# Performance work log

Measured on AMD Instinct MI355X. Metric: run time of the kernel, lower is better.

Reference implementation:

```python
import jax, jax.numpy as jnp
import numpy as np
from math import factorial, sqrt, pi

MAX_DEG = 4
CUTOFF = 5.0

# ---------- Clebsch-Gordan coefficients for real spherical harmonics ----------

def _cg_complex(j1, m1, j2, m2, j3, m3):
    if m1 + m2 != m3 or j3 < abs(j1 - j2) or j3 > j1 + j2:
        return 0.0
    f = factorial
    pre = sqrt((2 * j3 + 1) * f(j1 + j2 - j3) * f(j1 - j2 + j3) * f(-j1 + j2 + j3) / f(j1 + j2 + j3 + 1))
    pre *= sqrt(f(j1 + m1) * f(j1 - m1) * f(j2 + m2) * f(j2 - m2) * f(j3 + m3) * f(j3 - m3))
    s = 0.0
    for k in range(0, j1 + j2 + j3 + 1):
        t = [k, j1 + j2 - j3 - k, j1 - m1 - k, j2 + m2 - k, j3 - j2 + m1 + k, j3 - j1 - m2 + k]
        if min(t) < 0:
            continue
        s += (-1) ** k / (f(t[0]) * f(t[1]) * f(t[2]) * f(t[3]) * f(t[4]) * f(t[5]))
    return pre * s


def _u_matrix(l):
    # complex->real spherical-harmonic change of basis, U[m_real+l, mu+l]
    U = np.zeros((2 * l + 1, 2 * l + 1), dtype=np.complex128)
    U[l, l] = 1.0
    inv_sqrt2 = 1.0 / sqrt(2.0)
    for m in range(1, l + 1):
        U[l + m, l + m] = ((-1) ** m) * inv_sqrt2
        U[l + m, l - m] = inv_sqrt2
        U[l - m, l - m] = 1j * inv_sqrt2
        U[l - m, l + m] = -1j * ((-1) ** m) * inv_sqrt2
    return U


def _real_cg(l1, l2, l3):
    C = np.zeros((2 * l1 + 1, 2 * l2 + 1, 2 * l3 + 1), dtype=np.complex128)
    for m1 in range(-l1, l1 + 1):
        for m2 in range(-l2, l2 + 1):
            m3 = m1 + m2
            if -l3 <= m3 <= l3:
                C[m1 + l1, m2 + l2, m3 + l3] = _cg_complex(l1, m1, l2, m2, l3, m3)
    R = np.einsum('ai,bj,ck,ijk->abc', _u_matrix(l1), _u_matrix(l2), _u_matrix(l3).conj(), C)
    return np.real(R).astype(np.float32)

# Parity-even coupling paths (l1+l2+l3 even), all degrees <= MAX_DEG -> 42 paths
CG_PATHS = []
for _l1 in range(MAX_DEG + 1):
    for _l2 in range(MAX_DEG + 1):
        for _l3 in range(abs(_l1 - _l2), min(MAX_DEG, _l1 + _l2) + 1):
            if (_l1 + _l2 + _l3) % 2 == 0:
                CG_PATHS.append((_l1, _l2, _l3, _real_cg(_l1, _l2, _l3)))
NUM_PATHS = len(CG_PATHS)  # 42


def _sl(l):
    return slice(l * l, (l + 1) * (l + 1))


def tensor_product(x1, x2, w):
    # x1, x2: (E, 1, 25, F); w: (NUM_PATHS, F). One learnable weight per path per channel.
    blocks = [None] * (MAX_DEG + 1)
    for p, (l1, l2, l3, cg) in enumerate(CG_PATHS):
        a = x1[..., _sl(l1), :]
        b = x2[..., _sl(l2), :]
        c = jnp.einsum('...if,...jf,ijk->...kf', a, b, jnp.asarray(cg)) * w[p]
        blocks[l3] = c if blocks[l3] is None else blocks[l3] + c
    return jnp.concatenate(blocks, axis=-2)


def real_sph(u):
    # u: (E,3) unit vectors -> (E, 25) real orthonormal spherical harmonics, index l*l+l+m
    x, y, z = u[..., 0], u[..., 1], u[..., 2]
    L = MAX_DEG
    Cm = [jnp.ones_like(x)]
    Sm = [jnp.zeros_like(x)]
    for m in range(1, L + 1):
        Cm.append(x * Cm[m - 1] - y * Sm[m - 1])
        Sm.append(x * Sm[m - 1] + y * Cm[m - 1])
    Q = {(0, 0): jnp.ones_like(z)}
    for m in range(L + 1):
        if m > 0:
            Q[(m, m)] = (2 * m - 1) * Q[(m - 1, m - 1)]
        if m + 1 <= L:
            Q[(m + 1, m)] = (2 * m + 1) * z * Q[(m, m)]
        for l in range(m + 2, L + 1):
            Q[(l, m)] = ((2 * l - 1) * z * Q[(l - 1, m)] - (l + m - 1) * Q[(l - 2, m)]) / (l - m)
    ys = []
    for l in range(L + 1):
        row = [None] * (2 * l + 1)
        row[l] = sqrt((2 * l + 1) / (4 * pi)) * Q[(l, 0)]
        for m in range(1, l + 1):
            Klm = sqrt((2 * l + 1) / (4 * pi) * factorial(l - m) / factorial(l + m))
            base = sqrt(2.0) * Klm * Q[(l, m)]
            row[l + m] = base * Cm[m]
            row[l - m] = base * Sm[m]
        ys.extend(row)
    return jnp.stack(ys, axis=-1)


def bond_basis(disp, cutoff, num):
    # sinc radial basis * cosine cutoff * spherical harmonics -> (E, 1, 25, num)
    r = jnp.sqrt(jnp.sum(disp * disp, axis=-1) + 1e-12)
    Y = real_sph(disp / r[..., None])  # (E, 25)
    k = jnp.arange(1, num + 1, dtype=disp.dtype)
    rad = jnp.sinc(r[..., None] * k / cutoff)  # (E, num)
    cut = jnp.where(r < cutoff, 0.5 * (1.0 + jnp.cos(np.float32(np.pi) * r / cutoff)), 0.0)
    out = Y[..., :, None] * rad[..., None, :] * cut[..., None, None]
    return out[:, None, :, :]


def setup_inputs() -> dict:
    key = jax.random.key(0)
    k1, k2, k3, k4, k5, k6 = jax.random.split(key, 6)
    N, E, F = 10000, 160000, 16
    return {
        'atomic_descriptors': jax.random.normal(k1, (N, 1, 25, F), dtype=jnp.float32),
        'neighbour_displacements': jax.random.normal(k2, (E, 3), dtype=jnp.float32),
        'weights1': jax.random.normal(k3, (NUM_PATHS, F), dtype=jnp.float32),
        'weights2': jax.random.normal(k4, (NUM_PATHS, F), dtype=jnp.float32),
        'neighbours_i': jax.random.randint(k5, (E,), 0, N, dtype=jnp.int32),
        'neighbours_j': jax.random.randint(k6, (E,), 0, N, dtype=jnp.int32),
    }


def reference(atomic_descriptors, neighbour_displacements, weights1, weights2, neighbours_i, neighbours_j):
    F = atomic_descriptors.shape[-1]
    a1 = atomic_descriptors[neighbours_i]  # (E,1,25,F) irregular gather
    a2 = atomic_descriptors[neighbours_j]
    y = tensor_product(a1, a2, weights1)  # first equivariant CG tensor product
    bexp = bond_basis(neighbour_displacements, CUTOFF, F)  # radial x angular bond basis
    return tensor_product(y, bexp, weights2)
```

## Files before the change

### kernel.cpp

```cpp
#include <hip/hip_runtime.h>

namespace cg {

constexpr double FACT[16] = {
  1.0, 1.0, 2.0, 6.0, 24.0, 120.0, 720.0, 5040.0, 40320.0, 362880.0,
  3628800.0, 39916800.0, 479001600.0, 6227020800.0, 87178291200.0,
  1307674368000.0 };

constexpr double csqrt_(double x){
  if (x <= 0.0) return 0.0;
  double xx = x, g = 1.0;
  while (xx >= 256.0)      { xx *= (1.0/256.0); g *= 16.0;       }
  while (xx >= 4.0)        { xx *= 0.25;        g *= 2.0;        }
  while (xx < (1.0/256.0)) { xx *= 256.0;       g *= (1.0/16.0); }
  while (xx < 1.0)         { xx *= 4.0;         g *= 0.5;        }
  double s = 1.5;
  for (int i = 0; i < 10; ++i) s = 0.5*(s + xx/s);
  return g*s;
}

constexpr double cg_complex(int j1,int m1,int j2,int m2,int j3,int m3){
  if (m1+m2 != m3) return 0.0;
  int dj = j1-j2; if (dj < 0) dj = -dj;
  if (j3 < dj || j3 > j1+j2) return 0.0;
  if (m1<-j1||m1>j1||m2<-j2||m2>j2||m3<-j3||m3>j3) return 0.0;
  double pre = csqrt_((2.0*j3+1.0)*FACT[j1+j2-j3]*FACT[j1-j2+j3]*FACT[-j1+j2+j3]/FACT[j1+j2+j3+1]);
  pre *= csqrt_(FACT[j1+m1]*FACT[j1-m1]*FACT[j2+m2]*FACT[j2-m2]*FACT[j3+m3]*FACT[j3-m3]);
  double s = 0.0;
  for (int k = 0; k <= j1+j2+j3; ++k){
    int t1=j1+j2-j3-k, t2=j1-m1-k, t3=j2+m2-k, t4=j3-j2+m1+k, t5=j3-j1-m2+k;
    if (t1<0||t2<0||t3<0||t4<0||t5<0) continue;
    double term = 1.0/(FACT[k]*FACT[t1]*FACT[t2]*FACT[t3]*FACT[t4]*FACT[t5]);
    s += (k & 1) ? -term : term;
  }
  return pre*s;
}

struct URow { int n; int col[2]; double re[2]; double im[2]; };

constexpr URow urow(int l, int a){
  URow r{};
  const double is2 = 0.70710678118654752440;
  int m = a - l;
  if (m == 0){
    r.n = 1; r.col[0] = l; r.re[0] = 1.0; r.im[0] = 0.0;
  } else if (m > 0){
    r.n = 2;
    r.col[0] = l+m; r.re[0] = (m & 1) ? -is2 : is2; r.im[0] = 0.0;
    r.col[1] = l-m; r.re[1] = is2;                  r.im[1] = 0.0;
  } else {
    int mm = -m; r.n = 2;
    r.col[0] = l-mm; r.re[0] = 0.0; r.im[0] = is2;
    r.col[1] = l+mm; r.re[1] = 0.0; r.im[1] = (mm & 1) ? is2 : -is2;
  }
  return r;
}

struct PTab {
  int nnz;
  unsigned char ia[192];
  unsigned char jb[192];
  unsigned char kc[192];
  float v[192];
};

constexpr PTab build_path(int l1, int l2, int l3){
  double Cc[9][9] = {};
  for (int i = 0; i < 2*l1+1; ++i)
    for (int j = 0; j < 2*l2+1; ++j){
      int m3 = (i-l1)+(j-l2);
      Cc[i][j] = (m3 >= -l3 && m3 <= l3)
               ? cg_complex(l1, i-l1, l2, j-l2, l3, m3) : 0.0;
    }
  PTab t{};
  for (int a = 0; a < 2*l1+1; ++a)
    for (int b = 0; b < 2*l2+1; ++b)
      for (int c = 0; c < 2*l3+1; ++c){
        URow ra = urow(l1,a), rb = urow(l2,b), rc = urow(l3,c);
        double re = 0.0;
        for (int x = 0; x < ra.n; ++x)
          for (int yy = 0; yy < rb.n; ++yy){
            double pr = ra.re[x]*rb.re[yy] - ra.im[x]*rb.im[yy];
            double pi = ra.re[x]*rb.im[yy] + ra.im[x]*rb.re[yy];
            for (int z = 0; z < rc.n; ++z){
              if (rc.col[z]-l3 != (ra.col[x]-l1)+(rb.col[yy]-l2)) continue;
              double ure = pr*rc.re[z] + pi*rc.im[z];
              re += ure * Cc[ra.col[x]][rb.col[yy]];
            }
          }
        if (re > 1e-10 || re < -1e-10){
          t.ia[t.nnz] = (unsigned char)a;
          t.jb[t.nnz] = (unsigned char)b;
          t.kc[t.nnz] = (unsigned char)c;
          t.v[t.nnz]  = (float)re;
          t.nnz++;
        }
      }
  return t;
}

constexpr double PI_D = 3.14159265358979323846264338327950288;
constexpr double Kd(int l, int m){
  double v = csqrt_((2.0*l+1.0)/(4.0*PI_D)*FACT[l-m]/FACT[l+m]);
  if (m) v *= csqrt_(2.0);
  return v;
}

}

#define PATHS_X(X) \
  X(0,0,0,0) X(1,0,1,1) X(2,0,2,2) X(3,0,3,3) X(4,0,4,4) \
  X(5,1,0,1) X(6,1,1,0) X(7,1,1,2) X(8,1,2,1) X(9,1,2,3) X(10,1,3,2) X(11,1,3,4) X(12,1,4,3) \
  X(13,2,0,2) X(14,2,1,1) X(15,2,1,3) X(16,2,2,0) X(17,2,2,2) X(18,2,2,4) X(19,2,3,1) X(20,2,3,3) X(21,2,4,2) X(22,2,4,4) \
  X(23,3,0,3) X(24,3,1,2) X(25,3,1,4) X(26,3,2,1) X(27,3,2,3) X(28,3,3,0) X(29,3,3,2) X(30,3,3,4) X(31,3,4,1) X(32,3,4,3) \
  X(33,4,0,4) X(34,4,1,3) X(35,4,2,2) X(36,4,2,4) X(37,4,3,1) X(38,4,3,3) X(39,4,4,0) X(40,4,4,2) X(41,4,4,4)

#define DECL_TAB(P,L1,L2,L3) static constexpr cg::PTab CGT_##P = cg::build_path(L1,L2,L3);
PATHS_X(DECL_TAB)
#undef DECL_TAB

struct GTab {
  int n;
  int ptot;
  unsigned int zmask;
  unsigned char i8[512], j8[512], kk[512];
  bool np[512], ft[512];
  float v[512];
};

constexpr GTab merge_group(int npaths,
                           const cg::PTab* t0, int l30,
                           const cg::PTab* t1, int l31,
                           const cg::PTab* t2, int l32){
  GTab g{};
  const cg::PTab* ts[3] = {t0, t1, t2};
  int ls[3] = {l30, l31, l32};
  int pofs[3] = {0,0,0};
  int acc = 0;
  for (int s = 0; s < npaths; ++s){ pofs[s] = acc; acc += 2*ls[s]+1; }
  g.ptot = acc;
  bool touched[32] = {};
  for (int j = 0; j < 9; ++j)
    for (int i = 0; i < 9; ++i){
      bool first = true;
      for (int s = 0; s < npaths; ++s){
        const cg::PTab* T = ts[s];
        for (int t = 0; t < T->nnz; ++t){
          if ((int)T->ia[t] == i && (int)T->jb[t] == j){
            int kx = pofs[s] + (int)T->kc[t];
            g.i8[g.n] = (unsigned char)i;
            g.j8[g.n] = (unsigned char)j;
            g.kk[g.n] = (unsigned char)kx;
            g.np[g.n] = first; first = false;
            g.ft[g.n] = !touched[kx]; touched[kx] = true;
            g.v[g.n]  = T->v[t];
            g.n++;
          }
        }
      }
    }
  unsigned int zm = 0;
  for (int k = 0; k < g.ptot; ++k) if (!touched[k]) zm |= (1u << k);
  g.zmask = zm;
  return g;
}

#define GROUPS_X(X) \
  X(0,0, 1,  0,0,   0,0,   0,0) \
  X(0,1, 1,  1,1,   1,1,   1,1) \
  X(0,2, 1,  2,2,   2,2,   2,2) \
  X(0,3, 1,  3,3,   3,3,   3,3) \
  X(0,4, 1,  4,4,   4,4,   4,4) \
  X(1,0, 1,  5,1,   5,1,   5,1) \
  X(1,1, 2,  6,0,   7,2,   7,2) \
  X(1,2, 2,  8,1,   9,3,   9,3) \
  X(1,3, 2, 10,2,  11,4,  11,4) \
  X(1,4, 1, 12,3,  12,3,  12,3) \
  X(2,0, 1, 13,2,  13,2,  13,2) \
  X(2,1, 2, 14,1,  15,3,  15,3) \
  X(2,2, 3, 16,0,  17,2,  18,4) \
  X(2,3, 2, 19,1,  20,3,  20,3) \
  X(2,4, 2, 21,2,  22,4,  22,4) \
  X(3,0, 1, 23,3,  23,3,  23,3) \
  X(3,1, 2, 24,2,  25,4,  25,4) \
  X(3,2, 2, 26,1,  27,3,  27,3) \
  X(3,3, 3, 28,0,  29,2,  30,4) \
  X(3,4, 2, 31,1,  32,3,  32,3) \
  X(4,0, 1, 33,4,  33,4,  33,4) \
  X(4,1, 1, 34,3,  34,3,  34,3) \
  X(4,2, 2, 35,2,  36,4,  36,4) \
  X(4,3, 2, 37,1,  38,3,  38,3) \
  X(4,4, 3, 39,0,  40,2,  41,4)

#define DECL_GROUP(L1,L2,NP,P0,L30,P1,L31,P2,L32) \
  static constexpr GTab G_##L1##_##L2 = \
    merge_group(NP, &CGT_##P0, L30, &CGT_##P1, L31, &CGT_##P2, L32);
GROUPS_X(DECL_GROUP)
#undef DECL_GROUP

static constexpr float K00=(float)cg::Kd(0,0);
static constexpr float K10=(float)cg::Kd(1,0), K11=(float)cg::Kd(1,1);
static constexpr float K20=(float)cg::Kd(2,0), K21=(float)cg::Kd(2,1), K22=(float)cg::Kd(2,2);
static constexpr float K30=(float)cg::Kd(3,0), K31=(float)cg::Kd(3,1), K32=(float)cg::Kd(3,2), K33=(float)cg::Kd(3,3);
static constexpr float K40=(float)cg::Kd(4,0), K41=(float)cg::Kd(4,1), K42=(float)cg::Kd(4,2), K43=(float)cg::Kd(4,3), K44=(float)cg::Kd(4,4);

static constexpr float PI_F = 3.14159274101257324f;

#define RUN_GROUP(GN,L1,L2,NP,P0,L30,P1,L31,P2,L32,S1,S2,DST,WEX) { \
    float part[GN.ptot]; \
    _Pragma("unroll") \
    for (int k = 0; k < GN.ptot; ++k) if ((GN.zmask >> k) & 1u) part[k] = 0.f; \
    float prod = 0.f; \
    _Pragma("unroll") \
    for (int t = 0; t < GN.n; ++t) { \
      if (GN.np[t]) prod = S1[(L1)*(L1)+(int)GN.i8[t]] * S2[(L2)*(L2)+(int)GN.j8[t]]; \
      if (GN.ft[t]) part[GN.kk[t]]  = GN.v[t] * prod; \
      else          part[GN.kk[t]] += GN.v[t] * prod; \
    } \
    { const float wp = WEX(P0); \
      _Pragma("unroll") for (int k = 0; k < 2*(L30)+1; ++k) \
        DST[(L30)*(L30)+k] += wp * part[k]; } \
    if constexpr ((NP) > 1) { const float wp = WEX(P1); \
      _Pragma("unroll") for (int k = 0; k < 2*(L31)+1; ++k) \
        DST[(L31)*(L31)+k] += wp * part[2*(L30)+1 + k]; } \
    if constexpr ((NP) > 2) { const float wp = WEX(P2); \
      _Pragma("unroll") for (int k = 0; k < 2*(L32)+1; ++k) \
        DST[(L32)*(L32)+k] += wp * part[2*(L30)+1 + 2*(L31)+1 + k]; } \
  }

#define TP1W(P) (W1[(P)*16 + f])
#define TP2W(P) (s * W2[(P)*16 + f])

#define TP1_G(L1,L2,NP,P0,L30,P1,L31,P2,L32) \
  RUN_GROUP(G_##L1##_##L2, L1,L2,NP,P0,L30,P1,L31,P2,L32, a1,a2,y,TP1W)
#define TP2_G(L1,L2,NP,P0,L30,P1,L31,P2,L32) \
  RUN_GROUP(G_##L1##_##L2, L1,L2,NP,P0,L30,P1,L31,P2,L32, y,Ys,o,TP2W)

__global__ __launch_bounds__(256)
__attribute__((amdgpu_waves_per_eu(4, 4)))
void bctmd_kernel(
    const float* __restrict__ A,
    const float* __restrict__ D,
    const float* __restrict__ W1,
    const float* __restrict__ W2,
    const int*   __restrict__ NI,
    const int*   __restrict__ NJ,
    float* __restrict__ out,
    int E)
{
  int g = blockIdx.x * 256 + threadIdx.x;
  int e = g >> 4;
  int f = g & 15;
  if (e >= E) return;

  const float* __restrict__ a1p = A + (size_t)NI[e] * 400 + f;
  const float* __restrict__ a2p = A + (size_t)NJ[e] * 400 + f;

  float a1[25], a2[25];
#pragma unroll
  for (int i = 0; i < 25; ++i) a1[i] = a1p[i*16];
#pragma unroll
  for (int i = 0; i < 25; ++i) a2[i] = a2p[i*16];
#pragma unroll
  for (int i = 0; i < 25; ++i) { asm volatile("" : "+v"(a1[i])); }
#pragma unroll
  for (int i = 0; i < 25; ++i) { asm volatile("" : "+v"(a2[i])); }

  float y[25];
#pragma unroll
  for (int i = 0; i < 25; ++i) y[i] = 0.f;
  GROUPS_X(TP1_G)

  float dx = D[3*e], dy = D[3*e+1], dz = D[3*e+2];
  float r2 = dx*dx + dy*dy + dz*dz + 1e-12f;
  float inv = __builtin_amdgcn_rsqf(r2);
  float r   = r2 * inv;
  float ux = dx*inv, uy = dy*inv, uz = dz*inv;

  float Ys[25];
  {
    float C1 = ux,            S1 = uy;
    float C2 = ux*C1 - uy*S1, S2 = ux*S1 + uy*C1;
    float C3 = ux*C2 - uy*S2, S3 = ux*S2 + uy*C2;
    float C4 = ux*C3 - uy*S3, S4 = ux*S3 + uy*C3;
    float z = uz;
    float Q00 = 1.f;
    float Q11 = 1.f, Q22 = 3.f, Q33 = 15.f, Q44 = 105.f;
    float Q10 = z, Q21 = 3.f*z, Q32 = 15.f*z, Q43 = 105.f*z;
    float Q20 = 0.5f*(3.f*z*Q10 - Q00);
    float Q31 = 0.5f*(5.f*z*Q21 - 3.f*Q11);
    float Q42 = 0.5f*(7.f*z*Q32 - 5.f*Q22);
    float Q30 = (5.f*z*Q20 - 2.f*Q10)*(1.f/3.f);
    float Q41 = (7.f*z*Q31 - 4.f*Q21)*(1.f/3.f);
    float Q40 = 0.25f*(7.f*z*Q30 - 3.f*Q20);

    Ys[0]  = K00*Q00;
    Ys[1]  = K11*Q11*S1;  Ys[2]  = K10*Q10;     Ys[3]  = K11*Q11*C1;
    Ys[4]  = K22*Q22*S2;  Ys[5]  = K21*Q21*S1;  Ys[6]  = K20*Q20;
    Ys[7]  = K21*Q21*C1;  Ys[8]  = K22*Q22*C2;
    Ys[9]  = K33*Q33*S3;  Ys[10] = K32*Q32*S2;  Ys[11] = K31*Q31*S1;
    Ys[12] = K30*Q30;     Ys[13] = K31*Q31*C1;  Ys[14] = K32*Q32*C2;
    Ys[15] = K33*Q33*C3;
    Ys[16] = K44*Q44*S4;  Ys[17] = K43*Q43*S3;  Ys[18] = K42*Q42*S2;
    Ys[19] = K41*Q41*S1;  Ys[20] = K40*Q40;     Ys[21] = K41*Q41*C1;
    Ys[22] = K42*Q42*C2;  Ys[23] = K43*Q43*C3;  Ys[24] = K44*Q44*C4;
  }

  float base = PI_F * r * 0.2f;
  float tt  = base * (float)(f+1);
  float rad = __sinf(tt) * __builtin_amdgcn_rcpf(tt);
  float cut = (r < 5.0f) ? 0.5f*(1.0f + __cosf(base)) : 0.0f;
  float s   = rad * cut;

  float o[25];
#pragma unroll
  for (int i = 0; i < 25; ++i) o[i] = 0.f;
  GROUPS_X(TP2_G)

  float* __restrict__ op = out + (size_t)e * 400 + f;
#pragma unroll
  for (int k = 0; k < 25; ++k) op[k*16] = o[k];
}

extern "C" void kernel_launch(void* const* d_in, const int* in_sizes, int n_in,
                              void* d_out, int out_size, void* d_ws, size_t ws_size,
                              hipStream_t stream) {
  const float* A  = (const float*)d_in[0];
  const float* D  = (const float*)d_in[1];
  const float* W1 = (const float*)d_in[2];
  const float* W2 = (const float*)d_in[3];
  const int*   NI = (const int*)d_in[4];
  const int*   NJ = (const int*)d_in[5];
  float* out = (float*)d_out;

  int E = in_sizes[4];
  long total = (long)E * 16;
  int block = 256;
  int grid = (int)((total + block - 1) / block);
  bctmd_kernel<<<grid, block, 0, stream>>>(A, D, W1, W2, NI, NJ, out, E);
}
```

Baseline: 205.4 us.

## Pre-transpose atomic descriptors to per-channel contiguous layout for vectorized gathers

Adds a pre-pass kernel that rewrites the descriptor array into a workspace so that each (atom, channel) pair's 25 coefficients sit contiguously, padded to 28 floats. The main kernel then gathers them with float4 loads instead of 25 strided scalar loads per neighbour. The shared SH/TP2/store code is factored into a macro, and the asm register barriers are dropped from the fallback kernel. The cost is an extra kernel launch plus a write and read of a roughly 18 MB workspace, and the per-thread gathers are no longer coalesced across the 16 channels of an edge.

```diff
diff --git a/kernel.cpp b/kernel.cpp
--- a/kernel.cpp
+++ b/kernel.cpp
@@ -236,6 +236,111 @@
 #define TP2_G(L1,L2,NP,P0,L30,P1,L31,P2,L32) \
   RUN_GROUP(G_##L1##_##L2, L1,L2,NP,P0,L30,P1,L31,P2,L32, y,Ys,o,TP2W)
 
+#define SH_AND_TP2_AND_STORE() \
+  float dx = D[3*e], dy = D[3*e+1], dz = D[3*e+2]; \
+  float rr2 = dx*dx + dy*dy + dz*dz + 1e-12f; \
+  float rinv = __builtin_amdgcn_rsqf(rr2); \
+  float rr   = rr2 * rinv; \
+  float ux = dx*rinv, uy = dy*rinv, uz = dz*rinv; \
+  float Ys[25]; \
+  { \
+    float C1 = ux,            S1 = uy; \
+    float C2 = ux*C1 - uy*S1, S2 = ux*S1 + uy*C1; \
+    float C3 = ux*C2 - uy*S2, S3 = ux*S2 + uy*C2; \
+    float C4 = ux*C3 - uy*S3, S4 = ux*S3 + uy*C3; \
+    float z = uz; \
+    float Q00 = 1.f; \
+    float Q11 = 1.f, Q22 = 3.f, Q33 = 15.f, Q44 = 105.f; \
+    float Q10 = z, Q21 = 3.f*z, Q32 = 15.f*z, Q43 = 105.f*z; \
+    float Q20 = 0.5f*(3.f*z*Q10 - Q00); \
+    float Q31 = 0.5f*(5.f*z*Q21 - 3.f*Q11); \
+    float Q42 = 0.5f*(7.f*z*Q32 - 5.f*Q22); \
+    float Q30 = (5.f*z*Q20 - 2.f*Q10)*(1.f/3.f); \
+    float Q41 = (7.f*z*Q31 - 4.f*Q21)*(1.f/3.f); \
+    float Q40 = 0.25f*(7.f*z*Q30 - 3.f*Q20); \
+    Ys[0]  = K00*Q00; \
+    Ys[1]  = K11*Q11*S1;  Ys[2]  = K10*Q10;     Ys[3]  = K11*Q11*C1; \
+    Ys[4]  = K22*Q22*S2;  Ys[5]  = K21*Q21*S1;  Ys[6]  = K20*Q20; \
+    Ys[7]  = K21*Q21*C1;  Ys[8]  = K22*Q22*C2; \
+    Ys[9]  = K33*Q33*S3;  Ys[10] = K32*Q32*S2;  Ys[11] = K31*Q31*S1; \
+    Ys[12] = K30*Q30;     Ys[13] = K31*Q31*C1;  Ys[14] = K32*Q32*C2; \
+    Ys[15] = K33*Q33*C3; \
+    Ys[16] = K44*Q44*S4;  Ys[17] = K43*Q43*S3;  Ys[18] = K42*Q42*S2; \
+    Ys[19] = K41*Q41*S1;  Ys[20] = K40*Q40;     Ys[21] = K41*Q41*C1; \
+    Ys[22] = K42*Q42*C2;  Ys[23] = K43*Q43*C3;  Ys[24] = K44*Q44*C4; \
+  } \
+  float base = PI_F * rr * 0.2f; \
+  float tt  = base * (float)(f+1); \
+  float rad = __sinf(tt) * __builtin_amdgcn_rcpf(tt); \
+  float cut = (rr < 5.0f) ? 0.5f*(1.0f + __cosf(base)) : 0.0f; \
+  float s   = rad * cut; \
+  float o[25]; \
+  _Pragma("unroll") \
+  for (int i = 0; i < 25; ++i) o[i] = 0.f; \
+  GROUPS_X(TP2_G) \
+  float* __restrict__ op = out + (size_t)e * 400 + f; \
+  _Pragma("unroll") \
+  for (int k = 0; k < 25; ++k) op[k*16] = o[k];
+
+__global__ __launch_bounds__(256) void transpose_A(
+    const float* __restrict__ A, float* __restrict__ At, int N)
+{
+  int g = blockIdx.x * 256 + threadIdx.x;
+  if (g >= N * 16) return;
+  int n = g >> 4, f = g & 15;
+  const float* __restrict__ src = A + (size_t)n * 400 + f;
+  float* __restrict__ dst = At + (size_t)g * 28;
+  float v[25];
+#pragma unroll
+  for (int i = 0; i < 25; ++i) v[i] = src[i*16];
+#pragma unroll
+  for (int i = 0; i < 25; ++i) dst[i] = v[i];
+}
+
+__global__ __launch_bounds__(256)
+__attribute__((amdgpu_waves_per_eu(4, 4)))
+void bctmd_kernel_t(
+    const float* __restrict__ At,
+    const float* __restrict__ D,
+    const float* __restrict__ W1,
+    const float* __restrict__ W2,
+    const int*   __restrict__ NI,
+    const int*   __restrict__ NJ,
+    float* __restrict__ out,
+    int E)
+{
+  int g = blockIdx.x * 256 + threadIdx.x;
+  int e = g >> 4;
+  int f = g & 15;
+  if (e >= E) return;
+
+  const float4* __restrict__ p1 =
+      (const float4*)(At + ((size_t)NI[e] * 16 + f) * 28);
+  const float4* __restrict__ p2 =
+      (const float4*)(At + ((size_t)NJ[e] * 16 + f) * 28);
+
+  float a1[25], a2[25];
+#pragma unroll
+  for (int q = 0; q < 6; ++q) {
+    float4 t = p1[q];
+    a1[q*4+0] = t.x; a1[q*4+1] = t.y; a1[q*4+2] = t.z; a1[q*4+3] = t.w;
+  }
+  a1[24] = ((const float*)p1)[24];
+#pragma unroll
+  for (int q = 0; q < 6; ++q) {
+    float4 t = p2[q];
+    a2[q*4+0] = t.x; a2[q*4+1] = t.y; a2[q*4+2] = t.z; a2[q*4+3] = t.w;
+  }
+  a2[24] = ((const float*)p2)[24];
+
+  float y[25];
+#pragma unroll
+  for (int i = 0; i < 25; ++i) y[i] = 0.f;
+  GROUPS_X(TP1_G)
+
+  SH_AND_TP2_AND_STORE()
+}
+
 __global__ __launch_bounds__(256)
 __attribute__((amdgpu_waves_per_eu(4, 4)))
 void bctmd_kernel(
@@ -261,65 +366,13 @@
   for (int i = 0; i < 25; ++i) a1[i] = a1p[i*16];
 #pragma unroll
   for (int i = 0; i < 25; ++i) a2[i] = a2p[i*16];
-#pragma unroll
-  for (int i = 0; i < 25; ++i) { asm volatile("" : "+v"(a1[i])); }
-#pragma unroll
-  for (int i = 0; i < 25; ++i) { asm volatile("" : "+v"(a2[i])); }
 
   float y[25];
 #pragma unroll
   for (int i = 0; i < 25; ++i) y[i] = 0.f;
   GROUPS_X(TP1_G)
 
-  float dx = D[3*e], dy = D[3*e+1], dz = D[3*e+2];
-  float r2 = dx*dx + dy*dy + dz*dz + 1e-12f;
-  float inv = __builtin_amdgcn_rsqf(r2);
-  float r   = r2 * inv;
-  float ux = dx*inv, uy = dy*inv, uz = dz*inv;
-
-  float Ys[25];
-  {
-    float C1 = ux,            S1 = uy;
-    float C2 = ux*C1 - uy*S1, S2 = ux*S1 + uy*C1;
-    float C3 = ux*C2 - uy*S2, S3 = ux*S2 + uy*C2;
-    float C4 = ux*C3 - uy*S3, S4 = ux*S3 + uy*C3;
-    float z = uz;
-    float Q00 = 1.f;
-    float Q11 = 1.f, Q22 = 3.f, Q33 = 15.f, Q44 = 105.f;
-    float Q10 = z, Q21 = 3.f*z, Q32 = 15.f*z, Q43 = 105.f*z;
-    float Q20 = 0.5f*(3.f*z*Q10 - Q00);
-    float Q31 = 0.5f*(5.f*z*Q21 - 3.f*Q11);
-    float Q42 = 0.5f*(7.f*z*Q32 - 5.f*Q22);
-    float Q30 = (5.f*z*Q20 - 2.f*Q10)*(1.f/3.f);
-    float Q41 = (7.f*z*Q31 - 4.f*Q21)*(1.f/3.f);
-    float Q40 = 0.25f*(7.f*z*Q30 - 3.f*Q20);
-
-    Ys[0]  = K00*Q00;
-    Ys[1]  = K11*Q11*S1;  Ys[2]  = K10*Q10;     Ys[3]  = K11*Q11*C1;
-    Ys[4]  = K22*Q22*S2;  Ys[5]  = K21*Q21*S1;  Ys[6]  = K20*Q20;
-    Ys[7]  = K21*Q21*C1;  Ys[8]  = K22*Q22*C2;
-    Ys[9]  = K33*Q33*S3;  Ys[10] = K32*Q32*S2;  Ys[11] = K31*Q31*S1;
-    Ys[12] = K30*Q30;     Ys[13] = K31*Q31*C1;  Ys[14] = K32*Q32*C2;
-    Ys[15] = K33*Q33*C3;
-    Ys[16] = K44*Q44*S4;  Ys[17] = K43*Q43*S3;  Ys[18] = K42*Q42*S2;
-    Ys[19] = K41*Q41*S1;  Ys[20] = K40*Q40;     Ys[21] = K41*Q41*C1;
-    Ys[22] = K42*Q42*C2;  Ys[23] = K43*Q43*C3;  Ys[24] = K44*Q44*C4;
-  }
-
-  float base = PI_F * r * 0.2f;
-  float tt  = base * (float)(f+1);
-  float rad = __sinf(tt) * __builtin_amdgcn_rcpf(tt);
-  float cut = (r < 5.0f) ? 0.5f*(1.0f + __cosf(base)) : 0.0f;
-  float s   = rad * cut;
-
-  float o[25];
-#pragma unroll
-  for (int i = 0; i < 25; ++i) o[i] = 0.f;
-  GROUPS_X(TP2_G)
-
-  float* __restrict__ op = out + (size_t)e * 400 + f;
-#pragma unroll
-  for (int k = 0; k < 25; ++k) op[k*16] = o[k];
+  SH_AND_TP2_AND_STORE()
 }
 
 extern "C" void kernel_launch(void* const* d_in, const int* in_sizes, int n_in,
@@ -333,9 +386,19 @@
   const int*   NJ = (const int*)d_in[5];
   float* out = (float*)d_out;
 
+  int N = in_sizes[0] / 400;
   int E = in_sizes[4];
   long total = (long)E * 16;
   int block = 256;
   int grid = (int)((total + block - 1) / block);
-  bctmd_kernel<<<grid, block, 0, stream>>>(A, D, W1, W2, NI, NJ, out, E);
-}
+
+  size_t at_bytes = (size_t)N * 16 * 28 * sizeof(float);
+  if (ws_size >= at_bytes) {
+    float* At = (float*)d_ws;
+    int tgrid = (N * 16 + 255) / 256;
+    transpose_A<<<tgrid, 256, 0, stream>>>(A, At, N);
+    bctmd_kernel_t<<<grid, block, 0, stream>>>(At, D, W1, W2, NI, NJ, out, E);
+  } else {
+    bctmd_kernel<<<grid, block, 0, stream>>>(A, D, W1, W2, NI, NJ, out, E);
+  }
+}
```

New measurement: 223.4 us. 8.8% more time.
